# Kernel tuning notes

Measured on AMD Instinct MI355X. Metric: run time of the kernel, lower is better.

The kernel has to match this reference:

```python
import jax, jax.numpy as jnp
import numpy as np
import math

HIDDEN = 1024
HEADS = 16

def setup_inputs() -> dict:
    key = jax.random.key(0)
    k1, k2, k3 = jax.random.split(key, 3)
    B, T, C = 4, 2048, HIDDEN
    x = jax.random.normal(k1, (B, T, C), dtype=jnp.float32)
    w_qkv = jax.random.normal(k2, (C, 3 * C), dtype=jnp.float32) * (1.0 / math.sqrt(C))
    b_qkv = jnp.zeros((3 * C,), dtype=jnp.float32)
    w_out = jax.random.normal(k3, (C, C), dtype=jnp.float32) * (1.0 / math.sqrt(C))
    b_out = jnp.zeros((C,), dtype=jnp.float32)
    return {"x": x, "w_qkv": w_qkv, "b_qkv": b_qkv, "w_out": w_out, "b_out": b_out}

def reference(x, w_qkv, b_qkv, w_out, b_out):
    B, T, C = x.shape
    H = HEADS
    D = C // H  # head dim
    qkv = x @ w_qkv + b_qkv  # [B,T,3C]
    q, k, v = jnp.split(qkv, 3, axis=2)
    # [B,T,C] -> [B,H,T,D]
    q = q.reshape(B, T, H, D).transpose(0, 2, 1, 3)
    k = k.reshape(B, T, H, D).transpose(0, 2, 1, 3)
    v = v.reshape(B, T, H, D).transpose(0, 2, 1, 3)
    scale = 1.0 / math.sqrt(D)
    logits = jnp.einsum('bhqd,bhkd->bhqk', q, k) * scale  # [B,H,T,T]
    causal = jnp.tril(jnp.ones((T, T), dtype=bool))
    logits = jnp.where(causal[None, None, :, :], logits, -jnp.inf)
    probs = jax.nn.softmax(logits, axis=-1)
    out = jnp.einsum('bhqk,bhkd->bhqd', probs, v)  # [B,H,T,D]
    out = out.transpose(0, 2, 1, 3).reshape(B, T, C)
    return out @ w_out + b_out
```

## Files before the change

kernel.cpp:

```cpp
#include <hip/hip_runtime.h>
#include <hip/hip_bf16.h>

#define C_DIM  1024
#define NHEAD  16
#define DHEAD  64
#define T_LEN  2048
#define B_SZ   4
#define M_ROWS (B_SZ * T_LEN)
#define QKV_N  (3 * C_DIM)

typedef __bf16 bf16x8 __attribute__((ext_vector_type(8)));
typedef float  f32x4  __attribute__((ext_vector_type(4)));
typedef unsigned short ushort8_t __attribute__((ext_vector_type(8)));

__device__ __forceinline__ unsigned short f2bf(float f) {
    union { float f; unsigned int u; } v; v.f = f;
    unsigned int r = v.u + 0x7FFFu + ((v.u >> 16) & 1u);
    return (unsigned short)(r >> 16);
}

__device__ __forceinline__ bf16x8 as_bf16x8(ushort8_t u) {
    return __builtin_bit_cast(bf16x8, u);
}

__device__ __forceinline__ f32x4 mfma16(bf16x8 a, bf16x8 b, f32x4 c) {
    return __builtin_amdgcn_mfma_f32_16x16x32_bf16(a, b, c, 0, 0, 0);
}

__device__ __forceinline__ void block_sync_lds() {
    asm volatile("s_waitcnt lgkmcnt(0)" ::: "memory");
    __builtin_amdgcn_s_barrier();
}

#define GLL16(gsrc, ldst) __builtin_amdgcn_global_load_lds( \
    (const __attribute__((address_space(1))) void*)(gsrc),  \
    (__attribute__((address_space(3))) void*)(ldst), 16, 0, 0)

__device__ __forceinline__ int xcd_remap(int id, int nwg) {
    const int q = nwg >> 3, r = nwg & 7;
    const int xcd = id & 7, off = id >> 3;
    return (xcd < r) ? (xcd * (q + 1) + off) : (r * (q + 1) + (xcd - r) * q + off);
}

__global__ void k_convert(const float* __restrict__ in, unsigned short* __restrict__ out, int n4) {
    int i = blockIdx.x * blockDim.x + threadIdx.x;
    if (i >= n4) return;
    const float4 v = ((const float4*)in)[i];
    unsigned int lo = (unsigned int)f2bf(v.x) | ((unsigned int)f2bf(v.y) << 16);
    unsigned int hi = (unsigned int)f2bf(v.z) | ((unsigned int)f2bf(v.w) << 16);
    ((uint2*)out)[i] = make_uint2(lo, hi);
}

__global__ void k_transpose_bf16(const float* __restrict__ w, unsigned short* __restrict__ wT,
                                 int K, int N) {
    __shared__ float tile[32][33];
    const int n0 = blockIdx.x * 32, k0 = blockIdx.y * 32;
    const int tx = threadIdx.x, ty = threadIdx.y;
    for (int i = 0; i < 32; i += 8)
        tile[ty + i][tx] = w[(size_t)(k0 + ty + i) * N + (n0 + tx)];
    __syncthreads();
    for (int i = 0; i < 32; i += 8)
        wT[(size_t)(n0 + ty + i) * K + (k0 + tx)] = f2bf(tile[tx][ty + i]);
}

__global__ void k_transpose_v(const unsigned short* __restrict__ qkv,
                              unsigned short* __restrict__ vtg) {
    __shared__ unsigned short tile[32][33];
    const int tt = blockIdx.x;
    const int dy = blockIdx.y;
    const int bh = dy >> 1, dtile = dy & 1;
    const int b = bh >> 4, h = bh & 15;
    const int t0 = tt * 32, d0 = dtile * 32;
    const int tx = threadIdx.x, ty = threadIdx.y;
    const unsigned short* src = qkv + (size_t)b * T_LEN * QKV_N + 2 * C_DIM + h * DHEAD + d0;
    for (int i = 0; i < 32; i += 8)
        tile[ty + i][tx] = src[(size_t)(t0 + ty + i) * QKV_N + tx];
    __syncthreads();
    unsigned short* dst = vtg + ((size_t)bh * DHEAD + d0) * T_LEN + t0;
    for (int i = 0; i < 32; i += 8)
        dst[(size_t)(ty + i) * T_LEN + tx] = tile[tx][ty + i];
}

template<int BF16_OUT>
__global__ __launch_bounds__(256) void k_gemm(const unsigned short* __restrict__ A,
                       const unsigned short* __restrict__ Bt,
                       const float* __restrict__ bias,
                       void* __restrict__ C,
                       int M, int N, int K) {
    __shared__ unsigned short As[128][64];
    __shared__ unsigned short Bs[128][64];

    const int tid  = threadIdx.x;
    const int lane = tid & 63;
    const int wv   = tid >> 6;
    const int wm = wv >> 1, wn = wv & 1;

    const int nwg = gridDim.x * gridDim.y;
    const int wg  = xcd_remap(blockIdx.y * gridDim.x + blockIdx.x, nwg);
    const int bx = wg % gridDim.x, by = wg / gridDim.x;
    const int m0 = by * 128;
    const int n0 = bx * 128;
    const int lr = lane & 15, lg = lane >> 4;

    f32x4 acc[4][4];
#pragma unroll
    for (int i = 0; i < 4; i++)
#pragma unroll
        for (int j = 0; j < 4; j++) acc[i][j] = (f32x4){0.f, 0.f, 0.f, 0.f};

    const int gr = lane >> 3;
    const int gc = 8 * ((lane & 7) ^ gr);

    for (int kt = 0; kt < K; kt += 64) {
        __syncthreads();
#pragma unroll
        for (int j = 0; j < 4; j++) {
            const int row = 32 * wv + 8 * j;
            GLL16(A  + (size_t)(m0 + row + gr) * K + kt + gc, &As[row][0]);
            GLL16(Bt + (size_t)(n0 + row + gr) * K + kt + gc, &Bs[row][0]);
        }
        __syncthreads();

#pragma unroll
        for (int s = 0; s < 2; s++) {
            const int cb = (s * 64 + lg * 16) ^ ((lr & 7) << 4);
            bf16x8 af[4], bfr[4];
#pragma unroll
            for (int i = 0; i < 4; i++)
                af[i] = as_bf16x8(*(const ushort8_t*)((const char*)&As[wm * 64 + i * 16 + lr][0] + cb));
#pragma unroll
            for (int j = 0; j < 4; j++)
                bfr[j] = as_bf16x8(*(const ushort8_t*)((const char*)&Bs[wn * 64 + j * 16 + lr][0] + cb));
#pragma unroll
            for (int i = 0; i < 4; i++)
#pragma unroll
                for (int j = 0; j < 4; j++)
                    acc[i][j] = mfma16(af[i], bfr[j], acc[i][j]);
        }
    }

#pragma unroll
    for (int i = 0; i < 4; i++) {
#pragma unroll
        for (int j = 0; j < 4; j++) {
            const int col = n0 + wn * 64 + j * 16 + lr;
            const float bv = bias ? bias[col] : 0.f;
#pragma unroll
            for (int r = 0; r < 4; r++) {
                const int row = m0 + wm * 64 + i * 16 + lg * 4 + r;
                const float v = acc[i][j][r] + bv;
                if (BF16_OUT)
                    ((unsigned short*)C)[(size_t)row * N + col] = f2bf(v);
                else
                    ((float*)C)[(size_t)row * N + col] = v;
            }
        }
    }
}

#define KS_OFF(B_, ROW_) (((B_) << 13) + ((ROW_) << 7))
#define VS_OFF(B_, ROW_) (16384 + ((B_) << 13) + ((ROW_) << 7))
#define PL_OFF(W_)       (32768 + ((W_) << 11))
__global__ __launch_bounds__(256, 2) void k_attn(const unsigned short* __restrict__ qkv,
                                                 const unsigned short* __restrict__ vtg,
                                                 unsigned short* __restrict__ out) {
    __shared__ __align__(16) char smem[40960];

    const int blk = xcd_remap(blockIdx.x, B_SZ * NHEAD * 16);
    const int pr = blk & 15;
    const int h  = (blk >> 4) & 15;
    const int b  = blk >> 8;
    const int bh = b * 16 + h;

    const int tid  = threadIdx.x;
    const int lane = tid & 63;
    const int w    = tid >> 6;
    const int lr = lane & 15, lg = lane >> 4;
    const int gr = lane >> 3;
    const int gc = 8 * ((lane & 7) ^ gr);
    const int ra = w * 16;

    const size_t base = (size_t)b * T_LEN * QKV_N + (size_t)h * DHEAD;
    const unsigned short* Qp = qkv + base;
    const unsigned short* Kp = qkv + base + C_DIM;
    const unsigned short* Vt = vtg + (size_t)bh * DHEAD * T_LEN;

    int buf = 0;
    for (int t = 0; t < 2; t++) {
        const int qt = (t == 0) ? pr : (31 - pr);
        const int qw = qt * 64 + w * 16;
        const int R  = qt + 1;

        bf16x8 qf[2];
#pragma unroll
        for (int s = 0; s < 2; s++)
            qf[s] = as_bf16x8(*(const ushort8_t*)&Qp[(size_t)(qw + lr) * QKV_N + s * 32 + lg * 8]);

        f32x4 o[4];
#pragma unroll
        for (int f = 0; f < 4; f++) o[f] = (f32x4){0.f, 0.f, 0.f, 0.f};
        float lp[4] = {0.f, 0.f, 0.f, 0.f};

        GLL16(Kp + (size_t)(ra + gr) * QKV_N + gc,          smem + KS_OFF(buf, ra));
        GLL16(Kp + (size_t)(ra + 8 + gr) * QKV_N + gc,      smem + KS_OFF(buf, ra + 8));
        GLL16(Vt + (size_t)(ra + gr) * T_LEN + gc,          smem + VS_OFF(buf, ra));
        GLL16(Vt + (size_t)(ra + 8 + gr) * T_LEN + gc,      smem + VS_OFF(buf, ra + 8));

        for (int r = 0; r < R; ++r) {
            const int kb = r * 64;
            if (r + 1 < R) {
                const int kn = kb + 64;
                GLL16(Kp + (size_t)(kn + ra + gr) * QKV_N + gc,     smem + KS_OFF(buf ^ 1, ra));
                GLL16(Kp + (size_t)(kn + ra + 8 + gr) * QKV_N + gc, smem + KS_OFF(buf ^ 1, ra + 8));
                GLL16(Vt + (size_t)(ra + gr) * T_LEN + kn + gc,     smem + VS_OFF(buf ^ 1, ra));
                GLL16(Vt + (size_t)(ra + 8 + gr) * T_LEN + kn + gc, smem + VS_OFF(buf ^ 1, ra + 8));
                asm volatile("s_waitcnt vmcnt(4)" ::: "memory");
            } else {
                asm volatile("s_waitcnt vmcnt(0)" ::: "memory");
            }
            __builtin_amdgcn_s_barrier();
            __builtin_amdgcn_sched_barrier(0);

            f32x4 s4[4];
            __builtin_amdgcn_s_setprio(1);
#pragma unroll
            for (int f = 0; f < 4; f++) {
                const int row = f * 16 + lr;
                const bf16x8 kf0 = as_bf16x8(*(const ushort8_t*)
                    (smem + KS_OFF(buf, row) + ((lg * 16) ^ ((lr & 7) << 4))));
                const bf16x8 kf1 = as_bf16x8(*(const ushort8_t*)
                    (smem + KS_OFF(buf, row) + ((64 + lg * 16) ^ ((lr & 7) << 4))));
                f32x4 s = (f32x4){0.f, 0.f, 0.f, 0.f};
                s = mfma16(qf[0], kf0, s);
                s = mfma16(qf[1], kf1, s);
                s4[f] = s;
            }
            __builtin_amdgcn_s_setprio(0);

            const bool last = (r == R - 1);
#pragma unroll
            for (int rr = 0; rr < 4; rr++) {
                const int prow = lg * 4 + rr;
                const int qg = qw + prow;
                float part = 0.f;
#pragma unroll
                for (int f = 0; f < 4; f++) {
                    float sv = fminf(s4[f][rr] * 0.125f, 50.f);
                    if (last) {
                        const int kg = kb + f * 16 + lr;
                        if (kg > qg) sv = -1e30f;
                    }
                    const float e = __expf(sv);
                    part += e;
                    const int col = f * 16 + lr;
                    *(unsigned short*)(smem + PL_OFF(w) + prow * 128 +
                                       ((col * 2) ^ ((prow & 7) << 4))) = f2bf(e);
                }
                lp[rr] += part;
            }

            bf16x8 pa[2];
#pragma unroll
            for (int st = 0; st < 2; st++)
                pa[st] = as_bf16x8(*(const ushort8_t*)
                    (smem + PL_OFF(w) + lr * 128 + ((st * 64 + lg * 16) ^ ((lr & 7) << 4))));

            __builtin_amdgcn_s_setprio(1);
#pragma unroll
            for (int f = 0; f < 4; f++) {
                const int row = f * 16 + lr;
#pragma unroll
                for (int st = 0; st < 2; st++) {
                    const bf16x8 bv = as_bf16x8(*(const ushort8_t*)
                        (smem + VS_OFF(buf, row) + ((st * 64 + lg * 16) ^ ((lr & 7) << 4))));
                    o[f] = mfma16(pa[st], bv, o[f]);
                }
            }
            __builtin_amdgcn_s_setprio(0);

            block_sync_lds();
            buf ^= 1;
        }

#pragma unroll
        for (int rr = 0; rr < 4; rr++) {
            float v = lp[rr];
            v += __shfl_xor(v, 1, 64);
            v += __shfl_xor(v, 2, 64);
            v += __shfl_xor(v, 4, 64);
            v += __shfl_xor(v, 8, 64);
            lp[rr] = v;
        }

#pragma unroll
        for (int rr = 0; rr < 4; rr++) {
            const float inv = 1.f / lp[rr];
            const int q = qw + lg * 4 + rr;
#pragma unroll
            for (int f = 0; f < 4; f++)
                out[((size_t)b * T_LEN + q) * C_DIM + h * DHEAD + f * 16 + lr] =
                    f2bf(o[f][rr] * inv);
        }
    }
}

extern "C" void kernel_launch(void* const* d_in, const int* in_sizes, int n_in,
                              void* d_out, int out_size, void* d_ws, size_t ws_size,
                              hipStream_t stream) {
    const float* x      = (const float*)d_in[0];
    const float* w_qkv  = (const float*)d_in[1];
    const float* b_qkv  = (const float*)d_in[2];
    const float* w_out  = (const float*)d_in[3];
    const float* b_out  = (const float*)d_in[4];
    float* out = (float*)d_out;

    char* ws = (char*)d_ws;
    unsigned short* xb    = (unsigned short*)(ws);
    unsigned short* vtg   = (unsigned short*)(ws);
    unsigned short* wqkvT = (unsigned short*)(ws + 16777216);
    unsigned short* woutT = (unsigned short*)(ws + 16777216 + 6291456);
    unsigned short* qkv   = (unsigned short*)(ws + 25165824);
    unsigned short* attn  = (unsigned short*)(ws + 75497472);

    {
        const int n4 = M_ROWS * C_DIM / 4;
        k_convert<<<(n4 + 255) / 256, 256, 0, stream>>>(x, xb, n4);
    }
    k_transpose_bf16<<<dim3(QKV_N / 32, C_DIM / 32), dim3(32, 8), 0, stream>>>(w_qkv, wqkvT, C_DIM, QKV_N);
    k_transpose_bf16<<<dim3(C_DIM / 32, C_DIM / 32), dim3(32, 8), 0, stream>>>(w_out, woutT, C_DIM, C_DIM);
    k_gemm<1><<<dim3(QKV_N / 128, M_ROWS / 128), 256, 0, stream>>>(xb, wqkvT, b_qkv, qkv, M_ROWS, QKV_N, C_DIM);
    k_transpose_v<<<dim3(T_LEN / 32, 64 * 2), dim3(32, 8), 0, stream>>>(qkv, vtg);
    k_attn<<<B_SZ * NHEAD * 16, 256, 0, stream>>>(qkv, vtg, attn);
    k_gemm<0><<<dim3(C_DIM / 128, M_ROWS / 128), 256, 0, stream>>>(attn, woutT, b_out, out, M_ROWS, C_DIM, C_DIM);
}
```

Baseline: 180.4 us.

## Fuse V transpose into QKV GEMM epilogue and keep attention probs in registers

The QKV GEMM epilogue now writes the V columns directly in transposed per-head layout when the workspace is large enough, which removes the separate V-transpose kernel. The attention kernel computes S transposed (swapped MFMA operands), applies an exp2 with the scale folded in, and builds the P operand for the PV MFMA through cross-lane shuffles instead of an LDS round trip. This cuts the per-wave P buffer in LDS and reduces the row-sum reduction to two shuffles. The trade-off is extra shuffle instructions in the inner loop, plus a dependence on ws_size for the fused path.

```diff
diff --git a/kernel.cpp b/kernel.cpp
--- a/kernel.cpp
+++ b/kernel.cpp
@@ -12,6 +12,7 @@
 typedef __bf16 bf16x8 __attribute__((ext_vector_type(8)));
 typedef float  f32x4  __attribute__((ext_vector_type(4)));
 typedef unsigned short ushort8_t __attribute__((ext_vector_type(8)));
+typedef unsigned int   uint4_t   __attribute__((ext_vector_type(4)));
 
 __device__ __forceinline__ unsigned short f2bf(float f) {
     union { float f; unsigned int u; } v; v.f = f;
@@ -86,6 +87,7 @@
                        const unsigned short* __restrict__ Bt,
                        const float* __restrict__ bias,
                        void* __restrict__ C,
+                       unsigned short* __restrict__ vtg,
                        int M, int N, int K) {
     __shared__ unsigned short As[128][64];
     __shared__ unsigned short Bs[128][64];
@@ -139,20 +141,33 @@
         }
     }
 
+    const bool isV = (vtg != nullptr) && (n0 >= 2 * C_DIM);
 #pragma unroll
     for (int i = 0; i < 4; i++) {
 #pragma unroll
         for (int j = 0; j < 4; j++) {
             const int col = n0 + wn * 64 + j * 16 + lr;
             const float bv = bias ? bias[col] : 0.f;
-#pragma unroll
-            for (int r = 0; r < 4; r++) {
-                const int row = m0 + wm * 64 + i * 16 + lg * 4 + r;
-                const float v = acc[i][j][r] + bv;
-                if (BF16_OUT)
-                    ((unsigned short*)C)[(size_t)row * N + col] = f2bf(v);
-                else
-                    ((float*)C)[(size_t)row * N + col] = v;
+            if (isV) {
+                const int dcol = col - 2 * C_DIM;
+                const int hh = dcol >> 6, dd = dcol & 63;
+                const int row0 = m0 + wm * 64 + i * 16 + lg * 4;
+                const int bb = row0 >> 11, t0 = row0 & (T_LEN - 1);
+                const unsigned int p0 = (unsigned int)f2bf(acc[i][j][0] + bv)
+                                      | ((unsigned int)f2bf(acc[i][j][1] + bv) << 16);
+                const unsigned int p1 = (unsigned int)f2bf(acc[i][j][2] + bv)
+                                      | ((unsigned int)f2bf(acc[i][j][3] + bv) << 16);
+                *(uint2*)&vtg[(((size_t)(bb * 16 + hh)) * 64 + dd) * T_LEN + t0] = make_uint2(p0, p1);
+            } else {
+#pragma unroll
+                for (int r = 0; r < 4; r++) {
+                    const int row = m0 + wm * 64 + i * 16 + lg * 4 + r;
+                    const float v = acc[i][j][r] + bv;
+                    if (BF16_OUT)
+                        ((unsigned short*)C)[(size_t)row * N + col] = f2bf(v);
+                    else
+                        ((float*)C)[(size_t)row * N + col] = v;
+                }
             }
         }
     }
@@ -160,11 +175,11 @@
 
 #define KS_OFF(B_, ROW_) (((B_) << 13) + ((ROW_) << 7))
 #define VS_OFF(B_, ROW_) (16384 + ((B_) << 13) + ((ROW_) << 7))
-#define PL_OFF(W_)       (32768 + ((W_) << 11))
+#define SCALE2 0.180336880f
 __global__ __launch_bounds__(256, 2) void k_attn(const unsigned short* __restrict__ qkv,
                                                  const unsigned short* __restrict__ vtg,
                                                  unsigned short* __restrict__ out) {
-    __shared__ __align__(16) char smem[40960];
+    __shared__ __align__(16) char smem[32768];
 
     const int blk = xcd_remap(blockIdx.x, B_SZ * NHEAD * 16);
     const int pr = blk & 15;
@@ -180,6 +195,10 @@
     const int gc = 8 * ((lane & 7) ^ gr);
     const int ra = w * 16;
 
+    const int sA = lr + 32 * (lg & 1);
+    const int sB = sA + 16;
+    const int fhi = lg >> 1;
+
     const size_t base = (size_t)b * T_LEN * QKV_N + (size_t)h * DHEAD;
     const unsigned short* Qp = qkv + base;
     const unsigned short* Kp = qkv + base + C_DIM;
@@ -189,6 +208,7 @@
     for (int t = 0; t < 2; t++) {
         const int qt = (t == 0) ? pr : (31 - pr);
         const int qw = qt * 64 + w * 16;
+        const int qg = qw + lr;
         const int R  = qt + 1;
 
         bf16x8 qf[2];
@@ -199,7 +219,7 @@
         f32x4 o[4];
 #pragma unroll
         for (int f = 0; f < 4; f++) o[f] = (f32x4){0.f, 0.f, 0.f, 0.f};
-        float lp[4] = {0.f, 0.f, 0.f, 0.f};
+        float lp = 0.f;
 
         GLL16(Kp + (size_t)(ra + gr) * QKV_N + gc,          smem + KS_OFF(buf, ra));
         GLL16(Kp + (size_t)(ra + 8 + gr) * QKV_N + gc,      smem + KS_OFF(buf, ra + 8));
@@ -231,75 +251,78 @@
                 const bf16x8 kf1 = as_bf16x8(*(const ushort8_t*)
                     (smem + KS_OFF(buf, row) + ((64 + lg * 16) ^ ((lr & 7) << 4))));
                 f32x4 s = (f32x4){0.f, 0.f, 0.f, 0.f};
-                s = mfma16(qf[0], kf0, s);
-                s = mfma16(qf[1], kf1, s);
+                s = mfma16(kf0, qf[0], s);
+                s = mfma16(kf1, qf[1], s);
                 s4[f] = s;
             }
             __builtin_amdgcn_s_setprio(0);
 
             const bool last = (r == R - 1);
-#pragma unroll
-            for (int rr = 0; rr < 4; rr++) {
-                const int prow = lg * 4 + rr;
-                const int qg = qw + prow;
-                float part = 0.f;
-#pragma unroll
-                for (int f = 0; f < 4; f++) {
-                    float sv = fminf(s4[f][rr] * 0.125f, 50.f);
+            unsigned int Dk[4][2];
+#pragma unroll
+            for (int f = 0; f < 4; f++) {
+                unsigned short hh[4];
+#pragma unroll
+                for (int rr = 0; rr < 4; rr++) {
+                    float sv = fminf(s4[f][rr] * SCALE2, 72.f);
                     if (last) {
-                        const int kg = kb + f * 16 + lr;
+                        const int kg = kb + f * 16 + lg * 4 + rr;
                         if (kg > qg) sv = -1e30f;
                     }
-                    const float e = __expf(sv);
-                    part += e;
-                    const int col = f * 16 + lr;
-                    *(unsigned short*)(smem + PL_OFF(w) + prow * 128 +
-                                       ((col * 2) ^ ((prow & 7) << 4))) = f2bf(e);
+                    const float e = __builtin_amdgcn_exp2f(sv);
+                    lp += e;
+                    hh[rr] = __builtin_bit_cast(unsigned short, (__bf16)e);
                 }
-                lp[rr] += part;
-            }
-
-            bf16x8 pa[2];
-#pragma unroll
-            for (int st = 0; st < 2; st++)
-                pa[st] = as_bf16x8(*(const ushort8_t*)
-                    (smem + PL_OFF(w) + lr * 128 + ((st * 64 + lg * 16) ^ ((lr & 7) << 4))));
-
-            __builtin_amdgcn_s_setprio(1);
-#pragma unroll
-            for (int f = 0; f < 4; f++) {
-                const int row = f * 16 + lr;
-#pragma unroll
-                for (int st = 0; st < 2; st++) {
+                Dk[f][0] = (unsigned int)hh[0] | ((unsigned int)hh[1] << 16);
+                Dk[f][1] = (unsigned int)hh[2] | ((unsigned int)hh[3] << 16);
+            }
+
+#pragma unroll
+            for (int st = 0; st < 2; st++) {
+                const int a0 = __shfl((int)Dk[2 * st][0],     sA, 64);
+                const int b0 = __shfl((int)Dk[2 * st + 1][0], sA, 64);
+                const int a1 = __shfl((int)Dk[2 * st][1],     sA, 64);
+                const int b1 = __shfl((int)Dk[2 * st + 1][1], sA, 64);
+                const int a2 = __shfl((int)Dk[2 * st][0],     sB, 64);
+                const int b2 = __shfl((int)Dk[2 * st + 1][0], sB, 64);
+                const int a3 = __shfl((int)Dk[2 * st][1],     sB, 64);
+                const int b3 = __shfl((int)Dk[2 * st + 1][1], sB, 64);
+                uint4_t pw;
+                pw.x = (unsigned int)(fhi ? b0 : a0);
+                pw.y = (unsigned int)(fhi ? b1 : a1);
+                pw.z = (unsigned int)(fhi ? b2 : a2);
+                pw.w = (unsigned int)(fhi ? b3 : a3);
+                const bf16x8 pa = __builtin_bit_cast(bf16x8, pw);
+
+                __builtin_amdgcn_s_setprio(1);
+#pragma unroll
+                for (int f = 0; f < 4; f++) {
+                    const int row = f * 16 + lr;
                     const bf16x8 bv = as_bf16x8(*(const ushort8_t*)
                         (smem + VS_OFF(buf, row) + ((st * 64 + lg * 16) ^ ((lr & 7) << 4))));
-                    o[f] = mfma16(pa[st], bv, o[f]);
+                    o[f] = mfma16(pa, bv, o[f]);
                 }
-            }
-            __builtin_amdgcn_s_setprio(0);
+                __builtin_amdgcn_s_setprio(0);
+            }
 
             block_sync_lds();
             buf ^= 1;
         }
 
+        lp += __shfl_xor(lp, 16, 64);
+        lp += __shfl_xor(lp, 32, 64);
+
+        float inv[4];
+#pragma unroll
+        for (int rr = 0; rr < 4; rr++)
+            inv[rr] = 1.f / __shfl(lp, lg * 4 + rr, 64);
 #pragma unroll
         for (int rr = 0; rr < 4; rr++) {
-            float v = lp[rr];
-            v += __shfl_xor(v, 1, 64);
-            v += __shfl_xor(v, 2, 64);
-            v += __shfl_xor(v, 4, 64);
-            v += __shfl_xor(v, 8, 64);
-            lp[rr] = v;
-        }
-
-#pragma unroll
-        for (int rr = 0; rr < 4; rr++) {
-            const float inv = 1.f / lp[rr];
             const int q = qw + lg * 4 + rr;
 #pragma unroll
             for (int f = 0; f < 4; f++)
                 out[((size_t)b * T_LEN + q) * C_DIM + h * DHEAD + f * 16 + lr] =
-                    f2bf(o[f][rr] * inv);
+                    f2bf(o[f][rr] * inv[rr]);
         }
     }
 }
@@ -316,11 +339,15 @@
 
     char* ws = (char*)d_ws;
     unsigned short* xb    = (unsigned short*)(ws);
-    unsigned short* vtg   = (unsigned short*)(ws);
     unsigned short* wqkvT = (unsigned short*)(ws + 16777216);
     unsigned short* woutT = (unsigned short*)(ws + 16777216 + 6291456);
     unsigned short* qkv   = (unsigned short*)(ws + 25165824);
     unsigned short* attn  = (unsigned short*)(ws + 75497472);
+
+    const size_t VTG_OFF = 92274688ull;
+    const bool fused_vt = (ws_size >= VTG_OFF + 16777216ull);
+    unsigned short* vtg = fused_vt ? (unsigned short*)(ws + VTG_OFF)
+                                   : (unsigned short*)(ws);
 
     {
         const int n4 = M_ROWS * C_DIM / 4;
@@ -328,8 +355,11 @@
     }
     k_transpose_bf16<<<dim3(QKV_N / 32, C_DIM / 32), dim3(32, 8), 0, stream>>>(w_qkv, wqkvT, C_DIM, QKV_N);
     k_transpose_bf16<<<dim3(C_DIM / 32, C_DIM / 32), dim3(32, 8), 0, stream>>>(w_out, woutT, C_DIM, C_DIM);
-    k_gemm<1><<<dim3(QKV_N / 128, M_ROWS / 128), 256, 0, stream>>>(xb, wqkvT, b_qkv, qkv, M_ROWS, QKV_N, C_DIM);
-    k_transpose_v<<<dim3(T_LEN / 32, 64 * 2), dim3(32, 8), 0, stream>>>(qkv, vtg);
+    k_gemm<1><<<dim3(QKV_N / 128, M_ROWS / 128), 256, 0, stream>>>(
+        xb, wqkvT, b_qkv, qkv, fused_vt ? vtg : nullptr, M_ROWS, QKV_N, C_DIM);
+    if (!fused_vt)
+        k_transpose_v<<<dim3(T_LEN / 32, 64 * 2), dim3(32, 8), 0, stream>>>(qkv, vtg);
     k_attn<<<B_SZ * NHEAD * 16, 256, 0, stream>>>(qkv, vtg, attn);
-    k_gemm<0><<<dim3(C_DIM / 128, M_ROWS / 128), 256, 0, stream>>>(attn, woutT, b_out, out, M_ROWS, C_DIM, C_DIM);
-}
+    k_gemm<0><<<dim3(C_DIM / 128, M_ROWS / 128), 256, 0, stream>>>(
+        attn, woutT, b_out, out, nullptr, M_ROWS, C_DIM, C_DIM);
+}
```

After: 173.5 us. 1.04x faster.
